# Performance work log

Hardware: AMD Instinct MI355X
Metric: run time of the kernel (lower is better)

The kernel has to match this reference:

```python
import jax, jax.numpy as jnp
import numpy as np

B, N, C = 16, 577, 768
H, D = 12, 64
HID = 3072
EPS = 1e-5


def setup_inputs() -> dict:
    key = jax.random.key(0)
    ks = jax.random.split(key, 5)
    s = 0.02
    return {
        "x": jax.random.normal(ks[0], (B, N, C), jnp.float32),
        "w_qkv": jax.random.normal(ks[1], (C, 3 * C), jnp.float32) * s,
        "b_qkv": jnp.zeros((3 * C,), jnp.float32),
        "w_proj": jax.random.normal(ks[2], (C, C), jnp.float32) * s,
        "b_proj": jnp.zeros((C,), jnp.float32),
        "g1": jnp.ones((C,), jnp.float32),
        "be1": jnp.zeros((C,), jnp.float32),
        "g2": jnp.ones((C,), jnp.float32),
        "be2": jnp.zeros((C,), jnp.float32),
        "w1": jax.random.normal(ks[3], (C, HID), jnp.float32) * s,
        "b1": jnp.zeros((HID,), jnp.float32),
        "w2": jax.random.normal(ks[4], (HID, C), jnp.float32) * s,
        "b2": jnp.zeros((C,), jnp.float32),
    }


def _layernorm(x, g, b):
    mu = jnp.mean(x, axis=-1, keepdims=True)
    var = jnp.mean(jnp.square(x - mu), axis=-1, keepdims=True)
    return (x - mu) * jax.lax.rsqrt(var + EPS) * g + b


def reference(x, w_qkv, b_qkv, w_proj, b_proj, g1, be1, g2, be2, w1, b1, w2, b2):
    # --- pre-norm MHA ---
    xn = _layernorm(x, g1, be1)
    qkv = xn @ w_qkv + b_qkv                      # [B,N,3C]
    qkv = qkv.reshape(B, N, 3, H, D).transpose(2, 0, 3, 1, 4)  # [3,B,H,N,D]
    q, k, v = qkv[0], qkv[1], qkv[2]
    scale = 1.0 / jnp.sqrt(jnp.float32(D))
    scores = jnp.einsum("bhnd,bhmd->bhnm", q, k) * scale
    attn_weights = jax.nn.softmax(scores, axis=-1)  # [B,H,N,N]
    ctx = jnp.einsum("bhnm,bhmd->bhnd", attn_weights, v)
    ctx = ctx.transpose(0, 2, 1, 3).reshape(B, N, C)
    attn_out = ctx @ w_proj + b_proj
    x = x + attn_out
    # --- MLP (exact GELU, matching nn.GELU default) ---
    h = _layernorm(x, g2, be2) @ w1 + b1
    h = jax.nn.gelu(h, approximate=False)
    x = x + (h @ w2 + b2)
    return x, attn_weights
```

## Files before the change

kernel.cpp:

```cpp
#include <hip/hip_runtime.h>
#include <hip/hip_bf16.h>
#include <cmath>

constexpr int B_ = 16, N_ = 577, C_ = 768, H_ = 12, D_ = 64, HID_ = 3072;
constexpr int ROWS_ = B_ * N_;
constexpr int BH_ = B_ * H_;
constexpr int KVT_ = 10;
constexpr int QBLK_ = 10;

typedef __attribute__((ext_vector_type(8))) __bf16 bf16x8;
typedef __attribute__((ext_vector_type(4))) float f32x4;
typedef __attribute__((ext_vector_type(4), aligned(4))) float f32x4u;

#define DEVI __device__ __forceinline__

DEVI unsigned short f2bf(float f) {
  unsigned u = __float_as_uint(f);
  return (unsigned short)((u + 0x7fffu + ((u >> 16) & 1u)) >> 16);
}
DEVI float bf2f(unsigned short u) { return __uint_as_float(((unsigned)u) << 16); }

DEVI void gload16(const void* src, void* dst) {
  __builtin_amdgcn_global_load_lds(
      (const __attribute__((address_space(1))) char*)src,
      (__attribute__((address_space(3))) char*)dst, 16, 0, 0);
}
#define VMCNT0 asm volatile("s_waitcnt vmcnt(0)" ::: "memory")

__global__ __launch_bounds__(256) void cvtT_kernel(const float* __restrict__ in,
                                                   unsigned short* __restrict__ out,
                                                   int K, int N) {
  __shared__ float t[64][65];
  int n0 = blockIdx.x * 64, k0 = blockIdx.y * 64;
  int tx = threadIdx.x & 63, ty = threadIdx.x >> 6;
#pragma unroll
  for (int r = 0; r < 16; r++) {
    int kr = ty * 16 + r;
    t[kr][tx] = in[(long)(k0 + kr) * N + n0 + tx];
  }
  __syncthreads();
#pragma unroll
  for (int r = 0; r < 16; r++) {
    int nr = ty * 16 + r;
    out[(long)(n0 + nr) * K + k0 + tx] = f2bf(t[tx][nr]);
  }
}

__global__ __launch_bounds__(256) void ln_kernel(const float* __restrict__ x,
                                                 const float* __restrict__ g,
                                                 const float* __restrict__ be,
                                                 unsigned short* __restrict__ out) {
  int row = blockIdx.x;
  const float* xr = x + (long)row * C_;
  float v[3];
  float s = 0.f, s2 = 0.f;
#pragma unroll
  for (int j = 0; j < 3; j++) {
    int i = threadIdx.x + j * 256;
    v[j] = xr[i];
    s += v[j];
    s2 += v[j] * v[j];
  }
#pragma unroll
  for (int o = 32; o > 0; o >>= 1) {
    s += __shfl_down(s, o);
    s2 += __shfl_down(s2, o);
  }
  __shared__ float sh[8];
  int w = threadIdx.x >> 6;
  if ((threadIdx.x & 63) == 0) { sh[w] = s; sh[4 + w] = s2; }
  __syncthreads();
  s = sh[0] + sh[1] + sh[2] + sh[3];
  s2 = sh[4] + sh[5] + sh[6] + sh[7];
  float mu = s * (1.f / C_);
  float var = s2 * (1.f / C_) - mu * mu;
  float rs = rsqrtf(var + 1e-5f);
#pragma unroll
  for (int j = 0; j < 3; j++) {
    int i = threadIdx.x + j * 256;
    out[(long)row * C_ + i] = f2bf((v[j] - mu) * rs * g[i] + be[i]);
  }
}

__global__ __launch_bounds__(256) void attn_kernel(
    const unsigned short* __restrict__ qg,
    const unsigned short* __restrict__ kg,
    const unsigned short* __restrict__ vt,
    float* __restrict__ attn,
    unsigned short* __restrict__ ctx) {
  __shared__ unsigned short KVs[2][2][64][64];
  __shared__ unsigned short Ps[4][16][72];
  const int wgid = (blockIdx.x & 7) * (BH_ * QBLK_ / 8) + (blockIdx.x >> 3);
  const int bh = wgid / QBLK_, qb = wgid % QBLK_;
  const int b = bh / H_, h = bh % H_;
  const int tid = threadIdx.x, wave = tid >> 6, lane = tid & 63;
  const int l15 = lane & 15, l4 = lane >> 4;
  const int q0w = qb * 64 + wave * 16;

  const unsigned short* Qh = qg + (long)bh * N_ * D_;
  const char* Kb = (const char*)(kg + (long)bh * N_ * D_);
  const char* Vb = (const char*)(vt + (long)bh * D_ * N_);

  int qrc = q0w + l15; if (qrc >= N_) qrc = N_ - 1;
  bf16x8 qa0 = *(const bf16x8*)(Qh + (long)qrc * D_ + l4 * 8);
  bf16x8 qa1 = *(const bf16x8*)(Qh + (long)qrc * D_ + 32 + l4 * 8);

  auto stage = [&](int buf, int which, const char* g0, int rstride) {
#pragma unroll
    for (int i = 0; i < 2; i++) {
      int off = i * 4096 + tid * 16;
      int row = off >> 7, colD = off & 127;
      const char* src = g0 + (long)row * rstride + (colD ^ ((row & 7) << 4));
      char* dst = ((char*)KVs) + buf * 16384 + which * 8192 + i * 4096 + wave * 1024;
      gload16(src, dst);
    }
  };
  auto rdKV = [&](int buf, int which, int row, int colb) -> bf16x8 {
    const char* p = ((const char*)KVs) + buf * 16384 + which * 8192 + row * 128 +
                    (colb ^ ((row & 7) << 4));
    return *(const bf16x8*)p;
  };
  auto computeS = [&](int buf, int kv0, f32x4 (&s)[4]) {
#pragma unroll
    for (int nf = 0; nf < 4; nf++) {
      int row = nf * 16 + l15;
      bf16x8 k0v = rdKV(buf, 0, row, l4 * 16);
      bf16x8 k1v = rdKV(buf, 0, row, 64 + l4 * 16);
      f32x4 z = {0.f, 0.f, 0.f, 0.f};
      z = __builtin_amdgcn_mfma_f32_16x16x32_bf16(qa0, k0v, z, 0, 0, 0);
      z = __builtin_amdgcn_mfma_f32_16x16x32_bf16(qa1, k1v, z, 0, 0, 0);
      if (kv0 + row >= N_) z = f32x4{-1e30f, -1e30f, -1e30f, -1e30f};
      s[nf] = z;
    }
  };

  float m_ln[4], l_ln[4];
#pragma unroll
  for (int r = 0; r < 4; r++) { m_ln[r] = -1e30f; l_ln[r] = 0.f; }

  stage(0, 0, Kb, 128);
  VMCNT0; __syncthreads();
  int buf = 0;
  for (int kt = 0; kt < KVT_; kt++) {
    if (kt + 1 < KVT_) stage(buf ^ 1, 0, Kb + (long)(kt + 1) * 8192, 128);
    f32x4 s[4];
    computeS(buf, kt * 64, s);
#pragma unroll
    for (int r = 0; r < 4; r++) {
      float t0 = fmaxf(fmaxf(s[0][r], s[1][r]), fmaxf(s[2][r], s[3][r]));
      float mn = fmaxf(m_ln[r], t0);
      float sc = __expf(m_ln[r] - mn);
      l_ln[r] = l_ln[r] * sc + __expf(s[0][r] - mn) + __expf(s[1][r] - mn) +
                __expf(s[2][r] - mn) + __expf(s[3][r] - mn);
      m_ln[r] = mn;
    }
    VMCNT0; __syncthreads();
    buf ^= 1;
  }

  float m_run[4], inv_l[4];
#pragma unroll
  for (int r = 0; r < 4; r++) {
    float m = m_ln[r];
#pragma unroll
    for (int o = 1; o < 16; o <<= 1) m = fmaxf(m, __shfl_xor(m, o));
    float li = l_ln[r] * __expf(m_ln[r] - m);
#pragma unroll
    for (int o = 1; o < 16; o <<= 1) li += __shfl_xor(li, o);
    m_run[r] = m;
    inv_l[r] = 1.f / li;
  }

  f32x4 cacc[4];
#pragma unroll
  for (int nf = 0; nf < 4; nf++) cacc[nf] = f32x4{0.f, 0.f, 0.f, 0.f};

  stage(0, 0, Kb, 128);
  stage(0, 1, Vb, N_ * 2);
  VMCNT0; __syncthreads();
  buf = 0;
  for (int kt = 0; kt < KVT_; kt++) {
    const int kv0 = kt * 64;
    if (kt + 1 < KVT_) {
      stage(buf ^ 1, 0, Kb + (long)(kt + 1) * 8192, 128);
      stage(buf ^ 1, 1, Vb + (long)(kt + 1) * 128, N_ * 2);
    }
    f32x4 s[4];
    computeS(buf, kv0, s);
#pragma unroll
    for (int nf = 0; nf < 4; nf++)
#pragma unroll
      for (int r = 0; r < 4; r++) {
        float p = __expf(s[nf][r] - m_run[r]) * inv_l[r];
        Ps[wave][l4 * 4 + r][nf * 16 + l15] = f2bf(p);
      }
    if (kt < KVT_ - 1) {
      int prow = lane >> 4;
      int c0 = (lane & 15) * 4;
#pragma unroll
      for (int rg = 0; rg < 4; rg++) {
        int row = rg * 4 + prow;
        int qv = q0w + row;
        if (qv < N_) {
          ushort4 pb = *(const ushort4*)&Ps[wave][row][c0];
          f32x4u f;
          f[0] = bf2f(pb.x); f[1] = bf2f(pb.y); f[2] = bf2f(pb.z); f[3] = bf2f(pb.w);
          __builtin_nontemporal_store(
              f, (f32x4u*)(attn + ((long)bh * N_ + qv) * N_ + kv0 + c0));
        }
      }
    } else {
      if ((lane & 15) == 0) {
        int prow = lane >> 4;
#pragma unroll
        for (int rg = 0; rg < 4; rg++) {
          int row = rg * 4 + prow;
          int qv = q0w + row;
          if (qv < N_)
            __builtin_nontemporal_store(bf2f(Ps[wave][row][0]),
                                        attn + ((long)bh * N_ + qv) * N_ + 576);
        }
      }
    }
#pragma unroll
    for (int ks = 0; ks < 2; ks++) {
      bf16x8 pa = *(const bf16x8*)&Ps[wave][l15][ks * 32 + l4 * 8];
#pragma unroll
      for (int nf = 0; nf < 4; nf++) {
        bf16x8 vb = rdKV(buf, 1, nf * 16 + l15, ks * 64 + l4 * 16);
        cacc[nf] = __builtin_amdgcn_mfma_f32_16x16x32_bf16(pa, vb, cacc[nf], 0, 0, 0);
      }
    }
    VMCNT0; __syncthreads();
    buf ^= 1;
  }

#pragma unroll
  for (int nf = 0; nf < 4; nf++)
#pragma unroll
    for (int r = 0; r < 4; r++) {
      int qv = q0w + l4 * 4 + r;
      if (qv >= N_) continue;
      int d = nf * 16 + l15;
      ctx[((long)b * N_ + qv) * C_ + h * D_ + d] = f2bf(cacc[nf][r]);
    }
}

template <int EPI>
__global__ __launch_bounds__(256) void gemm128(
    const unsigned short* __restrict__ A,
    const unsigned short* __restrict__ BT,
    int M, int K, int Nc,
    void* __restrict__ outp, const float* __restrict__ bias,
    const float* __restrict__ resid) {
  __shared__ unsigned short As[2][128][64];
  __shared__ unsigned short Bs[2][128][64];
  const int tid = threadIdx.x, wave = tid >> 6, lane = tid & 63;
  const int l15 = lane & 15, l4 = lane >> 4;
  const long m0 = (long)blockIdx.y * 128, n0 = (long)blockIdx.x * 128;
  const int wr = (wave >> 1) * 64, wc = (wave & 1) * 64;

  f32x4 acc[4][4];
#pragma unroll
  for (int i = 0; i < 4; i++)
#pragma unroll
    for (int j = 0; j < 4; j++) acc[i][j] = f32x4{0.f, 0.f, 0.f, 0.f};

  auto stageA = [&](int buf, int t) {
#pragma unroll
    for (int i = 0; i < 4; i++) {
      int off = i * 4096 + tid * 16;
      int row = off >> 7, colD = off & 127;
      long gr = m0 + row; if (gr >= M) gr = M - 1;
      const char* src = (const char*)A + (gr * (long)K + (long)t * 64) * 2 +
                        (colD ^ ((row & 7) << 4));
      char* dst = ((char*)As) + buf * 16384 + i * 4096 + wave * 1024;
      gload16(src, dst);
    }
  };
  auto stageB = [&](int buf, int t) {
#pragma unroll
    for (int i = 0; i < 4; i++) {
      int off = i * 4096 + tid * 16;
      int row = off >> 7, colD = off & 127;
      const char* src = (const char*)BT + ((n0 + row) * (long)K + (long)t * 64) * 2 +
                        (colD ^ ((row & 7) << 4));
      char* dst = ((char*)Bs) + buf * 16384 + i * 4096 + wave * 1024;
      gload16(src, dst);
    }
  };

  const int nt = K / 64;
  stageA(0, 0); stageB(0, 0);
  VMCNT0; __syncthreads();
  int buf = 0;
  for (int t = 0; t < nt; t++) {
    if (t + 1 < nt) { stageA(buf ^ 1, t + 1); stageB(buf ^ 1, t + 1); }
    bf16x8 af[4][2], bfr[4][2];
#pragma unroll
    for (int mf = 0; mf < 4; mf++)
#pragma unroll
      for (int kk = 0; kk < 2; kk++) {
        int row = wr + mf * 16 + l15, colb = kk * 64 + l4 * 16;
        af[mf][kk] = *(const bf16x8*)(((const char*)As) + buf * 16384 + row * 128 +
                                      (colb ^ ((row & 7) << 4)));
      }
#pragma unroll
    for (int nf = 0; nf < 4; nf++)
#pragma unroll
      for (int kk = 0; kk < 2; kk++) {
        int row = wc + nf * 16 + l15, colb = kk * 64 + l4 * 16;
        bfr[nf][kk] = *(const bf16x8*)(((const char*)Bs) + buf * 16384 + row * 128 +
                                       (colb ^ ((row & 7) << 4)));
      }
#pragma unroll
    for (int kk = 0; kk < 2; kk++)
#pragma unroll
      for (int mf = 0; mf < 4; mf++)
#pragma unroll
        for (int nf = 0; nf < 4; nf++)
          acc[mf][nf] =
              __builtin_amdgcn_mfma_f32_16x16x32_bf16(af[mf][kk], bfr[nf][kk], acc[mf][nf], 0, 0, 0);
    VMCNT0; __syncthreads();
    buf ^= 1;
  }

#pragma unroll
  for (int mf = 0; mf < 4; mf++)
#pragma unroll
    for (int nf = 0; nf < 4; nf++)
#pragma unroll
      for (int r = 0; r < 4; r++) {
        long row = m0 + wr + mf * 16 + l4 * 4 + r;
        long col = n0 + wc + nf * 16 + l15;
        if (row >= M) continue;
        float v = acc[mf][nf][r];
        if constexpr (EPI == 0) {
          v += bias[col];
          int which = (int)col / C_;
          int rem = (int)col % C_;
          int hh = rem >> 6, d = rem & 63;
          int bb = (int)row / N_, n = (int)row % N_;
          if (which == 0) v *= 0.125f;
          unsigned short* o = (unsigned short*)outp;
          long base = (long)which * ((long)BH_ * N_ * D_);
          long idx;
          if (which < 2)
            idx = base + (((long)(bb * H_ + hh)) * N_ + n) * D_ + d;
          else
            idx = base + (((long)(bb * H_ + hh)) * D_ + d) * N_ + n;
          o[idx] = f2bf(v);
        } else if constexpr (EPI == 3 || EPI == 5) {
          float* o = (float*)outp;
          long idx = row * (long)Nc + col;
          o[idx] = v + bias[col] + resid[idx];
        } else if constexpr (EPI == 4) {
          v += bias[col];
          float ge = 0.5f * v * (1.f + erff(v * 0.70710678118654752f));
          ((unsigned short*)outp)[row * (long)Nc + col] = f2bf(ge);
        }
      }
}

extern "C" void kernel_launch(void* const* d_in, const int* in_sizes, int n_in,
                              void* d_out, int out_size, void* d_ws, size_t ws_size,
                              hipStream_t stream) {
  const float* x = (const float*)d_in[0];
  const float* w_qkv = (const float*)d_in[1];
  const float* b_qkv = (const float*)d_in[2];
  const float* w_proj = (const float*)d_in[3];
  const float* b_proj = (const float*)d_in[4];
  const float* g1 = (const float*)d_in[5];
  const float* be1 = (const float*)d_in[6];
  const float* g2 = (const float*)d_in[7];
  const float* be2 = (const float*)d_in[8];
  const float* w1 = (const float*)d_in[9];
  const float* b1 = (const float*)d_in[10];
  const float* w2 = (const float*)d_in[11];
  const float* b2 = (const float*)d_in[12];

  char* ws = (char*)d_ws;
  const size_t SZ_TOK_BF = (size_t)ROWS_ * C_ * 2;
  unsigned short* xn = (unsigned short*)(ws);
  unsigned short* q = (unsigned short*)(ws + SZ_TOK_BF);
  unsigned short* v = (unsigned short*)(ws + 3 * SZ_TOK_BF);
  unsigned short* ctx = (unsigned short*)(ws + 4 * SZ_TOK_BF);
  unsigned short* hbuf = q;
  float* x1 = (float*)(ws + 5 * SZ_TOK_BF);
  unsigned short* wqkvT = (unsigned short*)(ws + 5 * SZ_TOK_BF + (size_t)ROWS_ * C_ * 4);
  unsigned short* wprojT = wqkvT + (size_t)C_ * 3 * C_;
  unsigned short* w1T = wprojT + (size_t)C_ * C_;
  unsigned short* w2T = w1T + (size_t)C_ * HID_;

  float* out_x = (float*)d_out;
  float* attn = out_x + (size_t)ROWS_ * C_;

  cvtT_kernel<<<dim3(3 * C_ / 64, C_ / 64), 256, 0, stream>>>(w_qkv, wqkvT, C_, 3 * C_);
  cvtT_kernel<<<dim3(C_ / 64, C_ / 64), 256, 0, stream>>>(w_proj, wprojT, C_, C_);
  cvtT_kernel<<<dim3(HID_ / 64, C_ / 64), 256, 0, stream>>>(w1, w1T, C_, HID_);
  cvtT_kernel<<<dim3(C_ / 64, HID_ / 64), 256, 0, stream>>>(w2, w2T, HID_, C_);

  ln_kernel<<<ROWS_, 256, 0, stream>>>(x, g1, be1, xn);

  {
    dim3 g(3 * C_ / 128, (ROWS_ + 127) / 128);
    gemm128<0><<<g, 256, 0, stream>>>(xn, wqkvT, ROWS_, C_, 3 * C_, q, b_qkv, nullptr);
  }
  attn_kernel<<<BH_ * QBLK_, 256, 0, stream>>>(q, q + (size_t)BH_ * N_ * D_, v, attn, ctx);
  {
    dim3 g(C_ / 128, (ROWS_ + 127) / 128);
    gemm128<3><<<g, 256, 0, stream>>>(ctx, wprojT, ROWS_, C_, C_, x1, b_proj, x);
  }
  ln_kernel<<<ROWS_, 256, 0, stream>>>(x1, g2, be2, xn);
  {
    dim3 g(HID_ / 128, (ROWS_ + 127) / 128);
    gemm128<4><<<g, 256, 0, stream>>>(xn, w1T, ROWS_, C_, HID_, hbuf, b1, nullptr);
  }
  {
    dim3 g(C_ / 128, (ROWS_ + 127) / 128);
    gemm128<5><<<g, 256, 0, stream>>>(hbuf, w2T, ROWS_, HID_, C_, out_x, b2, x1);
  }
}
```

Baseline: 487.3 us.

## Add 256x256 pipelined GEMM for QKV and MLP-up projections

Adds a new 512-thread GEMM kernel with 256x256 output tiles, double-buffered swizzled LDS staging via direct global-to-LDS loads, interleaved prefetch per sub-phase, and an XCD-aware workgroup remap. The QKV and first MLP GEMMs use it in place of the 128x128 kernel. The goal is more data reuse per tile and better overlap of loads with MFMA work. The trade-off is higher register and LDS pressure and fewer workgroups, which leaves more of the last wave idle with M=9232.

```diff
diff --git a/kernel.cpp b/kernel.cpp
--- a/kernel.cpp
+++ b/kernel.cpp
@@ -26,6 +26,8 @@
       (__attribute__((address_space(3))) char*)dst, 16, 0, 0);
 }
 #define VMCNT0 asm volatile("s_waitcnt vmcnt(0)" ::: "memory")
+#define FENCE asm volatile("" ::: "memory")
+#define RAWBAR do { FENCE; __builtin_amdgcn_s_barrier(); FENCE; } while (0)
 
 __global__ __launch_bounds__(256) void cvtT_kernel(const float* __restrict__ in,
                                                    unsigned short* __restrict__ out,
@@ -335,22 +337,7 @@
         long col = n0 + wc + nf * 16 + l15;
         if (row >= M) continue;
         float v = acc[mf][nf][r];
-        if constexpr (EPI == 0) {
-          v += bias[col];
-          int which = (int)col / C_;
-          int rem = (int)col % C_;
-          int hh = rem >> 6, d = rem & 63;
-          int bb = (int)row / N_, n = (int)row % N_;
-          if (which == 0) v *= 0.125f;
-          unsigned short* o = (unsigned short*)outp;
-          long base = (long)which * ((long)BH_ * N_ * D_);
-          long idx;
-          if (which < 2)
-            idx = base + (((long)(bb * H_ + hh)) * N_ + n) * D_ + d;
-          else
-            idx = base + (((long)(bb * H_ + hh)) * D_ + d) * N_ + n;
-          o[idx] = f2bf(v);
-        } else if constexpr (EPI == 3 || EPI == 5) {
+        if constexpr (EPI == 3 || EPI == 5) {
           float* o = (float*)outp;
           long idx = row * (long)Nc + col;
           o[idx] = v + bias[col] + resid[idx];
@@ -360,6 +347,152 @@
           ((unsigned short*)outp)[row * (long)Nc + col] = f2bf(ge);
         }
       }
+}
+
+template <int EPI>
+__global__ __launch_bounds__(512, 2) void gemm256(
+    const unsigned short* __restrict__ A,
+    const unsigned short* __restrict__ BT,
+    int M, int K, int Nc,
+    void* __restrict__ outp, const float* __restrict__ bias,
+    const float* __restrict__ resid) {
+  __shared__ unsigned short smem[2][2][2][128][64];
+  const int tid = threadIdx.x, wave = tid >> 6, lane = tid & 63;
+  const int l15 = lane & 15, l4 = lane >> 4;
+  const int wm = wave >> 2, wn = wave & 3;
+
+  const int nbx = gridDim.x;
+  const int nwg = nbx * gridDim.y;
+  int orig = blockIdx.y * nbx + blockIdx.x;
+  int qq = nwg >> 3, r8 = nwg & 7;
+  int xcd = orig & 7, idx = orig >> 3;
+  int wg = (xcd < r8 ? xcd * (qq + 1) : r8 * (qq + 1) + (xcd - r8) * qq) + idx;
+  const long m0 = (long)(wg / nbx) * 256;
+  const long n0 = (long)(wg % nbx) * 256;
+
+  f32x4 acc[2][2][4][2];
+#pragma unroll
+  for (int a = 0; a < 2; a++)
+#pragma unroll
+    for (int b = 0; b < 2; b++)
+#pragma unroll
+      for (int m = 0; m < 4; m++)
+#pragma unroll
+        for (int n = 0; n < 2; n++) acc[a][b][m][n] = f32x4{0.f, 0.f, 0.f, 0.f};
+
+  auto stage = [&](int d, int op, int half, int t) {
+#pragma unroll
+    for (int it = 0; it < 2; it++) {
+      int off = it * 8192 + tid * 16;
+      int lrow = off >> 7, colb = off & 127;
+      long grow;
+      if (op == 0) {
+        grow = m0 + half * 128 + lrow;
+        if (grow >= M) grow = M - 1;
+      } else {
+        grow = n0 + half * 128 + lrow;
+      }
+      const unsigned short* gp = (op == 0) ? A : BT;
+      const char* src = (const char*)(gp + grow * (long)K + (long)t * 64) +
+                        (colb ^ ((lrow & 7) << 4));
+      char* dst = ((char*)smem) + (((d * 2 + op) * 2 + half) * 16384) + off;
+      gload16(src, dst);
+    }
+  };
+  auto rdfrag = [&](int d, int op, int half, int lr, int kk) -> bf16x8 {
+    const char* p = ((const char*)smem) + (((d * 2 + op) * 2 + half) * 16384) + lr * 128 +
+                    ((kk * 64 + l4 * 16) ^ ((lr & 7) << 4));
+    return *(const bf16x8*)p;
+  };
+
+  bf16x8 av[4][2];
+
+#define PHASE(d, qm, qn, STAGECODE, VMCODE)                                              \
+  {                                                                                      \
+    if constexpr (qn == 0) {                                                             \
+      _Pragma("unroll") for (int m = 0; m < 4; m++)                                      \
+          _Pragma("unroll") for (int kk = 0; kk < 2; kk++)                               \
+              av[m][kk] = rdfrag(d, 0, qm, wm * 64 + m * 16 + l15, kk);                  \
+    }                                                                                    \
+    bf16x8 bv[2][2];                                                                     \
+    _Pragma("unroll") for (int n = 0; n < 2; n++)                                        \
+        _Pragma("unroll") for (int kk = 0; kk < 2; kk++)                                 \
+            bv[n][kk] = rdfrag(d, 1, qn, wn * 32 + n * 16 + l15, kk);                    \
+    STAGECODE;                                                                           \
+    VMCODE;                                                                              \
+    RAWBAR;                                                                              \
+    __builtin_amdgcn_s_setprio(1);                                                       \
+    _Pragma("unroll") for (int kk = 0; kk < 2; kk++)                                     \
+        _Pragma("unroll") for (int m = 0; m < 4; m++)                                    \
+            _Pragma("unroll") for (int n = 0; n < 2; n++)                                \
+                acc[qm][qn][m][n] = __builtin_amdgcn_mfma_f32_16x16x32_bf16(             \
+                    av[m][kk], bv[n][kk], acc[qm][qn][m][n], 0, 0, 0);                   \
+    __builtin_amdgcn_s_setprio(0);                                                       \
+    RAWBAR;                                                                              \
+  }
+
+  const int nt = K / 64, ni = nt / 2;
+  stage(0, 0, 0, 0); stage(0, 0, 1, 0); stage(0, 1, 0, 0); stage(0, 1, 1, 0);
+  stage(1, 0, 0, 1); stage(1, 0, 1, 1); stage(1, 1, 0, 1); stage(1, 1, 1, 1);
+  asm volatile("s_waitcnt vmcnt(8)" ::: "memory");
+  RAWBAR;
+
+  for (int i = 0; i < ni; i++) {
+    const int t1 = 2 * i + 1, t2 = 2 * i + 2, t3 = 2 * i + 3;
+    PHASE(0, 0, 0, { if (i > 0) stage(1, 0, 1, t1); }, {});
+    PHASE(0, 0, 1, { if (i > 0) stage(1, 1, 1, t1); }, {});
+    PHASE(0, 1, 0, { if (t2 < nt) stage(0, 0, 0, t2); }, {});
+    PHASE(0, 1, 1, { if (t2 < nt) stage(0, 1, 0, t2); },
+          { if (t2 < nt) { asm volatile("s_waitcnt vmcnt(4)" ::: "memory"); }
+            else { asm volatile("s_waitcnt vmcnt(0)" ::: "memory"); } });
+    PHASE(1, 0, 0, { if (t2 < nt) stage(0, 0, 1, t2); }, {});
+    PHASE(1, 0, 1, { if (t2 < nt) stage(0, 1, 1, t2); }, {});
+    PHASE(1, 1, 0, { if (t3 < nt) stage(1, 0, 0, t3); }, {});
+    PHASE(1, 1, 1, { if (t3 < nt) stage(1, 1, 0, t3); },
+          { if (t3 < nt) { asm volatile("s_waitcnt vmcnt(4)" ::: "memory"); }
+            else { asm volatile("s_waitcnt vmcnt(0)" ::: "memory"); } });
+  }
+#undef PHASE
+
+#pragma unroll
+  for (int qm = 0; qm < 2; qm++)
+#pragma unroll
+    for (int qn = 0; qn < 2; qn++)
+#pragma unroll
+      for (int m = 0; m < 4; m++)
+#pragma unroll
+        for (int n = 0; n < 2; n++)
+#pragma unroll
+          for (int r = 0; r < 4; r++) {
+            long row = m0 + qm * 128 + wm * 64 + m * 16 + l4 * 4 + r;
+            long col = n0 + qn * 128 + wn * 32 + n * 16 + l15;
+            if (row >= M) continue;
+            float v = acc[qm][qn][m][n][r];
+            if constexpr (EPI == 0) {
+              v += bias[col];
+              int which = (int)col / C_;
+              int rem = (int)col % C_;
+              int hh = rem >> 6, d = rem & 63;
+              int bb = (int)row / N_, nn = (int)row % N_;
+              if (which == 0) v *= 0.125f;
+              unsigned short* o = (unsigned short*)outp;
+              long base = (long)which * ((long)BH_ * N_ * D_);
+              long oidx;
+              if (which < 2)
+                oidx = base + (((long)(bb * H_ + hh)) * N_ + nn) * D_ + d;
+              else
+                oidx = base + (((long)(bb * H_ + hh)) * D_ + d) * N_ + nn;
+              o[oidx] = f2bf(v);
+            } else if constexpr (EPI == 4) {
+              v += bias[col];
+              float ge = 0.5f * v * (1.f + erff(v * 0.70710678118654752f));
+              ((unsigned short*)outp)[row * (long)Nc + col] = f2bf(ge);
+            } else {
+              float* o = (float*)outp;
+              long oidx = row * (long)Nc + col;
+              o[oidx] = v + bias[col] + resid[oidx];
+            }
+          }
 }
 
 extern "C" void kernel_launch(void* const* d_in, const int* in_sizes, int n_in,
@@ -403,8 +536,8 @@
   ln_kernel<<<ROWS_, 256, 0, stream>>>(x, g1, be1, xn);
 
   {
-    dim3 g(3 * C_ / 128, (ROWS_ + 127) / 128);
-    gemm128<0><<<g, 256, 0, stream>>>(xn, wqkvT, ROWS_, C_, 3 * C_, q, b_qkv, nullptr);
+    dim3 g(3 * C_ / 256, (ROWS_ + 255) / 256);
+    gemm256<0><<<g, 512, 0, stream>>>(xn, wqkvT, ROWS_, C_, 3 * C_, q, b_qkv, nullptr);
   }
   attn_kernel<<<BH_ * QBLK_, 256, 0, stream>>>(q, q + (size_t)BH_ * N_ * D_, v, attn, ctx);
   {
@@ -413,8 +546,8 @@
   }
   ln_kernel<<<ROWS_, 256, 0, stream>>>(x1, g2, be2, xn);
   {
-    dim3 g(HID_ / 128, (ROWS_ + 127) / 128);
-    gemm128<4><<<g, 256, 0, stream>>>(xn, w1T, ROWS_, C_, HID_, hbuf, b1, nullptr);
+    dim3 g(HID_ / 256, (ROWS_ + 255) / 256);
+    gemm256<4><<<g, 512, 0, stream>>>(xn, w1T, ROWS_, C_, HID_, hbuf, b1, nullptr);
   }
   {
     dim3 g(C_ / 128, (ROWS_ + 127) / 128);
```

Result: no change. 490.1 us (+0.6%).
